# Optimization experiments

Measured on AMD Instinct MI355X. Metric: run time of the kernel, lower is better.

## Reference

```python
import jax, jax.numpy as jnp
import numpy as np

N = 8192
IN_C = 512
OUT_C = 512


def setup_inputs() -> dict:
    key = jax.random.key(0)
    k1, k2, k3 = jax.random.split(key, 3)
    x = jax.random.normal(k1, (N, IN_C), dtype=jnp.float32)
    adj = jax.random.uniform(k2, (N, N), dtype=jnp.float32)
    # torch.rand initializer for the weight (uniform [0,1))
    w = jax.random.uniform(k3, (IN_C, OUT_C), dtype=jnp.float32)
    return {"x": x, "adj": adj, "w": w}


def reference(x, adj, w):
    # A = adj + I
    A = adj + jnp.eye(adj.shape[0], dtype=adj.dtype)
    # D_hat = diag(deg)^{-1/2}; diagonal inverse + sqrt == elementwise rsqrt of degrees
    deg = jnp.sum(A, axis=1)                      # [N]
    d_inv_sqrt = jax.lax.rsqrt(deg)               # [N]
    # A_hat = D_hat @ A @ D_hat == row/col scaling (same math, no dense inverse)
    A_hat = A * d_inv_sqrt[:, None] * d_inv_sqrt[None, :]
    mm_1 = A_hat @ x                              # [N, in_c]
    return jax.nn.elu(mm_1 @ w)                   # [N, out_c]
```

## Files before the change

### kernel.cpp

```cpp
#include <hip/hip_runtime.h>

#define NN 8192
#define CC 512

typedef __attribute__((ext_vector_type(8))) short short8;
typedef __attribute__((ext_vector_type(4))) float f32x4;
typedef unsigned short ushort_t;

__device__ __forceinline__ unsigned short f2bf(float f) {
    unsigned int u = __float_as_uint(f);
    u += 0x7FFF + ((u >> 16) & 1);
    return (unsigned short)(u >> 16);
}

__device__ __forceinline__ void gload_lds16(const void* g, void* l) {
    __builtin_amdgcn_global_load_lds((const __attribute__((address_space(1))) unsigned int*)g,
                                     (__attribute__((address_space(3))) unsigned int*)l,
                                     16, 0, 0);
}

__global__ __launch_bounds__(256) void k_rowsum(const float* __restrict__ adj,
                                                float* __restrict__ ds) {
    int row = blockIdx.x;
    const float4* p = (const float4*)(adj + (size_t)row * NN);
    float s = 0.f;
#pragma unroll
    for (int i = 0; i < 8; ++i) {
        float4 v = p[threadIdx.x + i * 256];
        s += (v.x + v.y) + (v.z + v.w);
    }
#pragma unroll
    for (int off = 32; off > 0; off >>= 1) s += __shfl_down(s, off, 64);
    __shared__ float partial[4];
    int wid = threadIdx.x >> 6;
    int lane = threadIdx.x & 63;
    if (lane == 0) partial[wid] = s;
    __syncthreads();
    if (threadIdx.x == 0) {
        float deg = ((partial[0] + partial[1]) + (partial[2] + partial[3])) + 1.0f;
        ds[row] = rsqrtf(deg);
    }
}

__global__ __launch_bounds__(256) void k_transpose(const float* __restrict__ in,
                                                   ushort_t* __restrict__ out,
                                                   const float* __restrict__ scale,
                                                   int R, int C) {
    __shared__ float tile[64][65];
    int r0 = blockIdx.x * 64, c0 = blockIdx.y * 64;
    int t = threadIdx.x;
    int cl = t & 63;
    int rl0 = t >> 6;
#pragma unroll
    for (int i = 0; i < 16; ++i) {
        int r = rl0 + i * 4;
        float v = in[(size_t)(r0 + r) * C + c0 + cl];
        float sc = scale ? scale[r0 + r] : 1.0f;
        tile[r][cl] = v * sc;
    }
    __syncthreads();
#pragma unroll
    for (int i = 0; i < 16; ++i) {
        int c = rl0 + i * 4;
        int r = cl;
        out[(size_t)(c0 + c) * R + r0 + r] = f2bf(tile[r][c]);
    }
}

template <int MODE>
__global__ __launch_bounds__(256, 4) void k_gemm1(const float* __restrict__ adj,
                                                  const ushort_t* __restrict__ yt,
                                                  const float* __restrict__ ds,
                                                  const float* __restrict__ x,
                                                  ushort_t* __restrict__ mm1,
                                                  float* __restrict__ part) {
    __shared__ __align__(16) ushort_t As[128 * 64];
    __shared__ __align__(16) ushort_t Bs[128 * 64];

    int t = threadIdx.x;
    int wid = t >> 6, lane = t & 63;

    int rowBase, colBase, kt0, ktN, ks;
    if (MODE == 0) {
        int bid = blockIdx.x;
        bid = (bid & 7) * 32 + (bid >> 3);
        colBase = (bid & 3) * 128;
        rowBase = (bid >> 2) * 128;
        kt0 = 0; ktN = NN / 64; ks = 0;
    } else {
        int gid = blockIdx.x;
        int xcd = gid & 7, slot = gid >> 3;
        int cb = slot & 3;
        int g = (slot >> 2) * 8 + xcd;
        int rb = g & 63; ks = g >> 6;
        rowBase = rb * 128; colBase = cb * 128;
        kt0 = ks * (NN / 64 / 4); ktN = kt0 + NN / 64 / 4;
    }

    int ar = t >> 4;
    int ac4 = t & 15;
    const float* aptr = adj + (size_t)(rowBase + ar) * NN + ac4 * 4;

    int brow0 = t >> 3;
    int bs = t & 7;

    float4 areg[8];

    auto loadA = [&](int kt) {
        const float* p = aptr + kt * 64;
#pragma unroll
        for (int i = 0; i < 8; ++i)
            areg[i] = *(const float4*)(p + (size_t)i * 16 * NN);
    };
    auto writeA = [&]() {
#pragma unroll
        for (int i = 0; i < 8; ++i) {
            int row = i * 16 + ar;
            ushort4 u;
            u.x = f2bf(areg[i].x); u.y = f2bf(areg[i].y);
            u.z = f2bf(areg[i].z); u.w = f2bf(areg[i].w);
            *(ushort4*)((char*)As + row * 128 + ((ac4 * 8) ^ ((row & 7) << 4))) = u;
        }
    };
    auto stageB = [&](int kt) {
#pragma unroll
        for (int j = 0; j < 4; ++j) {
            int row = j * 32 + brow0;
            const char* g = (const char*)(yt + (size_t)(colBase + row) * NN + kt * 64 +
                                          ((bs ^ (row & 7)) << 3));
            char* l = (char*)Bs + j * 4096 + wid * 1024;
            gload_lds16(g, l);
        }
    };

    f32x4 acc[4][4] = {};
    int wr = wid >> 1, wc = wid & 1;
    int fr = lane & 15, fq = lane >> 4;

    loadA(kt0);
    for (int kt = kt0; kt < ktN; ++kt) {
        writeA();
        stageB(kt);
        __syncthreads();
        if (kt + 1 < ktN) loadA(kt + 1);
#pragma unroll
        for (int ks2 = 0; ks2 < 2; ++ks2) {
            short8 af[4], bf[4];
#pragma unroll
            for (int m = 0; m < 4; ++m) {
                int row = wr * 64 + m * 16 + fr;
                af[m] = *(const short8*)((const char*)As + row * 128 +
                                         ((ks2 * 64 + fq * 16) ^ ((row & 7) << 4)));
            }
#pragma unroll
            for (int n = 0; n < 4; ++n) {
                int col = wc * 64 + n * 16 + fr;
                bf[n] = *(const short8*)((const char*)Bs + col * 128 +
                                         ((ks2 * 64 + fq * 16) ^ ((col & 7) << 4)));
            }
#pragma unroll
            for (int m = 0; m < 4; ++m)
#pragma unroll
                for (int n = 0; n < 4; ++n)
                    acc[m][n] = __builtin_amdgcn_mfma_f32_16x16x32_bf16(af[m], bf[n], acc[m][n], 0, 0, 0);
        }
        __syncthreads();
    }

#pragma unroll
    for (int m = 0; m < 4; ++m) {
#pragma unroll
        for (int j = 0; j < 4; ++j) {
            int gr = rowBase + wr * 64 + m * 16 + fq * 4 + j;
            float dsr = (MODE == 0) ? ds[gr] : 0.f;
#pragma unroll
            for (int n = 0; n < 4; ++n) {
                int gc = colBase + wc * 64 + n * 16 + fr;
                float p = acc[m][n][j];
                if (MODE == 0) {
                    float v = dsr * (p + dsr * x[(size_t)gr * CC + gc]);
                    mm1[(size_t)gr * CC + gc] = f2bf(v);
                } else if (MODE == 1) {
                    part[((size_t)ks * NN + gr) * CC + gc] = p;
                } else {
                    atomicAdd(&part[(size_t)gr * CC + gc], p);
                }
            }
        }
    }
}

__global__ __launch_bounds__(256) void k_finish(const float* __restrict__ part,
                                                const float* __restrict__ ds,
                                                const float* __restrict__ x,
                                                ushort_t* __restrict__ mm1,
                                                int nsplit) {
    size_t i = (size_t)blockIdx.x * 256 + threadIdx.x;
    const f32x4* p = (const f32x4*)part;
    const size_t stride = (size_t)NN * CC / 4;
    f32x4 s = p[i];
    for (int k = 1; k < nsplit; ++k) s += p[i + (size_t)k * stride];
    int row = (int)(i >> 7);
    float d = ds[row];
    f32x4 xv = ((const f32x4*)x)[i];
    ushort4 u;
    u.x = f2bf(d * (s[0] + d * xv[0]));
    u.y = f2bf(d * (s[1] + d * xv[1]));
    u.z = f2bf(d * (s[2] + d * xv[2]));
    u.w = f2bf(d * (s[3] + d * xv[3]));
    ((ushort4*)mm1)[i] = u;
}

__global__ __launch_bounds__(256, 2) void k_gemm2(const ushort_t* __restrict__ mm1,
                                                  const ushort_t* __restrict__ wt,
                                                  float* __restrict__ out) {
    __shared__ __align__(16) ushort_t As[128 * 64];
    __shared__ __align__(16) ushort_t Bs[128 * 64];

    int t = threadIdx.x;
    int wid = t >> 6, lane = t & 63;
    int bid = blockIdx.x;
    bid = (bid & 7) * 32 + (bid >> 3);
    int cb = bid & 3, rb = bid >> 2;
    int rowBase = rb * 128, colBase = cb * 128;

    int srow0 = t >> 3, ss = t & 7;

    f32x4 acc[4][4] = {};
    int wr = wid >> 1, wc = wid & 1;
    int fr = lane & 15, fq = lane >> 4;

    for (int kt = 0; kt < CC / 64; ++kt) {
#pragma unroll
        for (int j = 0; j < 4; ++j) {
            int row = j * 32 + srow0;
            gload_lds16((const char*)(mm1 + (size_t)(rowBase + row) * CC + kt * 64 +
                                      ((ss ^ (row & 7)) << 3)),
                        (char*)As + j * 4096 + wid * 1024);
            gload_lds16((const char*)(wt + (size_t)(colBase + row) * CC + kt * 64 +
                                      ((ss ^ (row & 7)) << 3)),
                        (char*)Bs + j * 4096 + wid * 1024);
        }
        __syncthreads();
#pragma unroll
        for (int ks = 0; ks < 2; ++ks) {
            short8 af[4], bf[4];
#pragma unroll
            for (int m = 0; m < 4; ++m) {
                int row = wr * 64 + m * 16 + fr;
                af[m] = *(const short8*)((const char*)As + row * 128 +
                                         ((ks * 64 + fq * 16) ^ ((row & 7) << 4)));
            }
#pragma unroll
            for (int n = 0; n < 4; ++n) {
                int col = wc * 64 + n * 16 + fr;
                bf[n] = *(const short8*)((const char*)Bs + col * 128 +
                                         ((ks * 64 + fq * 16) ^ ((col & 7) << 4)));
            }
#pragma unroll
            for (int m = 0; m < 4; ++m)
#pragma unroll
                for (int n = 0; n < 4; ++n)
                    acc[m][n] = __builtin_amdgcn_mfma_f32_16x16x32_bf16(af[m], bf[n], acc[m][n], 0, 0, 0);
        }
        __syncthreads();
    }

#pragma unroll
    for (int m = 0; m < 4; ++m) {
#pragma unroll
        for (int j = 0; j < 4; ++j) {
            int gr = rowBase + wr * 64 + m * 16 + fq * 4 + j;
#pragma unroll
            for (int n = 0; n < 4; ++n) {
                int gc = colBase + wc * 64 + n * 16 + fr;
                float v = acc[m][n][j];
                out[(size_t)gr * CC + gc] = v > 0.f ? v : expm1f(v);
            }
        }
    }
}

extern "C" void kernel_launch(void* const* d_in, const int* in_sizes, int n_in,
                              void* d_out, int out_size, void* d_ws, size_t ws_size,
                              hipStream_t stream) {
    const float* x   = (const float*)d_in[0];
    const float* adj = (const float*)d_in[1];
    const float* w   = (const float*)d_in[2];
    float* out = (float*)d_out;

    char* ws = (char*)d_ws;
    size_t off = 0;
    float*    ds  = (float*)(ws + off);  off += 32u << 10;
    ushort_t* yt  = (ushort_t*)(ws + off);  off += 8u << 20;
    ushort_t* wt  = (ushort_t*)(ws + off);  off += 512u << 10;
    ushort_t* mm1 = (ushort_t*)(ws + off);  off += 8u << 20;
    float*    part = (float*)(ws + off);
    const size_t oneBuf = (size_t)NN * CC * 4;

    k_rowsum<<<NN, 256, 0, stream>>>(adj, ds);
    k_transpose<<<dim3(NN / 64, CC / 64), 256, 0, stream>>>(x, yt, ds, NN, CC);
    k_transpose<<<dim3(CC / 64, CC / 64), 256, 0, stream>>>(w, wt, nullptr, CC, CC);

    if (ws_size >= off + 4 * oneBuf) {
        k_gemm1<1><<<1024, 256, 0, stream>>>(adj, yt, ds, x, mm1, part);
        k_finish<<<NN * CC / 4 / 256, 256, 0, stream>>>(part, ds, x, mm1, 4);
    } else if (ws_size >= off + oneBuf) {
        hipMemsetAsync(part, 0, oneBuf, stream);
        k_gemm1<2><<<1024, 256, 0, stream>>>(adj, yt, ds, x, mm1, part);
        k_finish<<<NN * CC / 4 / 256, 256, 0, stream>>>(part, ds, x, mm1, 1);
    } else {
        k_gemm1<0><<<256, 256, 0, stream>>>(adj, yt, ds, x, mm1, part);
    }

    k_gemm2<<<256, 256, 0, stream>>>(mm1, wt, out);
}
```

Before: 220.5 us.

## Convert adjacency to bf16 during row-sum and stream it via direct LDS loads

The row-sum pass now also writes a bf16 copy of the adjacency matrix. A new split-K GEMM kernel then loads both operands with global_load_lds DMA instead of a register-staged fp32 load, convert and LDS write. This removes the in-loop conversion and register pressure from the main GEMM, but adds an extra 128MB write and a 128MB bf16 re-read on top of the 256MB fp32 read. The atomic fallback path is dropped, and the new path only runs when the workspace can hold the bf16 adjacency.

```diff
diff --git a/kernel.cpp b/kernel.cpp
--- a/kernel.cpp
+++ b/kernel.cpp
@@ -17,6 +17,32 @@
     __builtin_amdgcn_global_load_lds((const __attribute__((address_space(1))) unsigned int*)g,
                                      (__attribute__((address_space(3))) unsigned int*)l,
                                      16, 0, 0);
+}
+
+__global__ __launch_bounds__(256) void k_rowsum_cvt(const float* __restrict__ adj,
+                                                    float* __restrict__ ds,
+                                                    ushort_t* __restrict__ adj16) {
+    int row = blockIdx.x;
+    const float4* p = (const float4*)(adj + (size_t)row * NN);
+    ushort4* q = (ushort4*)(adj16 + (size_t)row * NN);
+    float s = 0.f;
+#pragma unroll
+    for (int i = 0; i < 8; ++i) {
+        float4 v = p[threadIdx.x + i * 256];
+        s += (v.x + v.y) + (v.z + v.w);
+        ushort4 u;
+        u.x = f2bf(v.x); u.y = f2bf(v.y); u.z = f2bf(v.z); u.w = f2bf(v.w);
+        q[threadIdx.x + i * 256] = u;
+    }
+#pragma unroll
+    for (int off = 32; off > 0; off >>= 1) s += __shfl_down(s, off, 64);
+    __shared__ float partial[4];
+    if ((threadIdx.x & 63) == 0) partial[threadIdx.x >> 6] = s;
+    __syncthreads();
+    if (threadIdx.x == 0) {
+        float deg = ((partial[0] + partial[1]) + (partial[2] + partial[3])) + 1.0f;
+        ds[row] = rsqrtf(deg);
+    }
 }
 
 __global__ __launch_bounds__(256) void k_rowsum(const float* __restrict__ adj,
@@ -32,9 +58,7 @@
 #pragma unroll
     for (int off = 32; off > 0; off >>= 1) s += __shfl_down(s, off, 64);
     __shared__ float partial[4];
-    int wid = threadIdx.x >> 6;
-    int lane = threadIdx.x & 63;
-    if (lane == 0) partial[wid] = s;
+    if ((threadIdx.x & 63) == 0) partial[threadIdx.x >> 6] = s;
     __syncthreads();
     if (threadIdx.x == 0) {
         float deg = ((partial[0] + partial[1]) + (partial[2] + partial[3])) + 1.0f;
@@ -64,6 +88,79 @@
         int c = rl0 + i * 4;
         int r = cl;
         out[(size_t)(c0 + c) * R + r0 + r] = f2bf(tile[r][c]);
+    }
+}
+
+__global__ __launch_bounds__(256, 4) void k_gemm1b(const ushort_t* __restrict__ adj16,
+                                                   const ushort_t* __restrict__ yt,
+                                                   float* __restrict__ part) {
+    __shared__ __align__(16) ushort_t As[128 * 64];
+    __shared__ __align__(16) ushort_t Bs[128 * 64];
+
+    int t = threadIdx.x;
+    int wid = t >> 6, lane = t & 63;
+
+    int gid = blockIdx.x;
+    int xcd = gid & 7, slot = gid >> 3;
+    int cb = slot & 3;
+    int g = (slot >> 2) * 8 + xcd;
+    int rb = g & 63, ks = g >> 6;
+    int rowBase = rb * 128, colBase = cb * 128;
+    int kt0 = ks * (NN / 64 / 4), ktN = kt0 + NN / 64 / 4;
+
+    int srow0 = t >> 3, ss = t & 7;
+
+    f32x4 acc[4][4] = {};
+    int wr = wid >> 1, wc = wid & 1;
+    int fr = lane & 15, fq = lane >> 4;
+
+    for (int kt = kt0; kt < ktN; ++kt) {
+#pragma unroll
+        for (int j = 0; j < 4; ++j) {
+            int row = j * 32 + srow0;
+            gload_lds16((const char*)(adj16 + (size_t)(rowBase + row) * NN + kt * 64 +
+                                      ((ss ^ (row & 7)) << 3)),
+                        (char*)As + j * 4096 + wid * 1024);
+            gload_lds16((const char*)(yt + (size_t)(colBase + row) * NN + kt * 64 +
+                                      ((ss ^ (row & 7)) << 3)),
+                        (char*)Bs + j * 4096 + wid * 1024);
+        }
+        __syncthreads();
+#pragma unroll
+        for (int ks2 = 0; ks2 < 2; ++ks2) {
+            short8 af[4], bf[4];
+#pragma unroll
+            for (int m = 0; m < 4; ++m) {
+                int row = wr * 64 + m * 16 + fr;
+                af[m] = *(const short8*)((const char*)As + row * 128 +
+                                         ((ks2 * 64 + fq * 16) ^ ((row & 7) << 4)));
+            }
+#pragma unroll
+            for (int n = 0; n < 4; ++n) {
+                int col = wc * 64 + n * 16 + fr;
+                bf[n] = *(const short8*)((const char*)Bs + col * 128 +
+                                         ((ks2 * 64 + fq * 16) ^ ((col & 7) << 4)));
+            }
+#pragma unroll
+            for (int m = 0; m < 4; ++m)
+#pragma unroll
+                for (int n = 0; n < 4; ++n)
+                    acc[m][n] = __builtin_amdgcn_mfma_f32_16x16x32_bf16(af[m], bf[n], acc[m][n], 0, 0, 0);
+        }
+        __syncthreads();
+    }
+
+#pragma unroll
+    for (int m = 0; m < 4; ++m) {
+#pragma unroll
+        for (int j = 0; j < 4; ++j) {
+            int gr = rowBase + wr * 64 + m * 16 + fq * 4 + j;
+#pragma unroll
+            for (int n = 0; n < 4; ++n) {
+                int gc = colBase + wc * 64 + n * 16 + fr;
+                part[((size_t)ks * NN + gr) * CC + gc] = acc[m][n][j];
+            }
+        }
     }
 }
 
@@ -100,7 +197,6 @@
     int ar = t >> 4;
     int ac4 = t & 15;
     const float* aptr = adj + (size_t)(rowBase + ar) * NN + ac4 * 4;
-
     int brow0 = t >> 3;
     int bs = t & 7;
 
@@ -126,10 +222,9 @@
 #pragma unroll
         for (int j = 0; j < 4; ++j) {
             int row = j * 32 + brow0;
-            const char* g = (const char*)(yt + (size_t)(colBase + row) * NN + kt * 64 +
-                                          ((bs ^ (row & 7)) << 3));
-            char* l = (char*)Bs + j * 4096 + wid * 1024;
-            gload_lds16(g, l);
+            gload_lds16((const char*)(yt + (size_t)(colBase + row) * NN + kt * 64 +
+                                      ((bs ^ (row & 7)) << 3)),
+                        (char*)Bs + j * 4096 + wid * 1024);
         }
     };
 
@@ -180,10 +275,8 @@
                 if (MODE == 0) {
                     float v = dsr * (p + dsr * x[(size_t)gr * CC + gc]);
                     mm1[(size_t)gr * CC + gc] = f2bf(v);
-                } else if (MODE == 1) {
+                } else {
                     part[((size_t)ks * NN + gr) * CC + gc] = p;
-                } else {
-                    atomicAdd(&part[(size_t)gr * CC + gc], p);
                 }
             }
         }
@@ -296,20 +389,26 @@
     ushort_t* wt  = (ushort_t*)(ws + off);  off += 512u << 10;
     ushort_t* mm1 = (ushort_t*)(ws + off);  off += 8u << 20;
     float*    part = (float*)(ws + off);
-    const size_t oneBuf = (size_t)NN * CC * 4;
-
-    k_rowsum<<<NN, 256, 0, stream>>>(adj, ds);
-    k_transpose<<<dim3(NN / 64, CC / 64), 256, 0, stream>>>(x, yt, ds, NN, CC);
-    k_transpose<<<dim3(CC / 64, CC / 64), 256, 0, stream>>>(w, wt, nullptr, CC, CC);
-
-    if (ws_size >= off + 4 * oneBuf) {
+    const size_t partBytes = 4 * (size_t)NN * CC * 4;
+    ushort_t* adj16 = (ushort_t*)(ws + off + partBytes);
+    const size_t adjBytes = (size_t)NN * NN * 2;
+
+    if (ws_size >= off + partBytes + adjBytes) {
+        k_rowsum_cvt<<<NN, 256, 0, stream>>>(adj, ds, adj16);
+        k_transpose<<<dim3(NN / 64, CC / 64), 256, 0, stream>>>(x, yt, ds, NN, CC);
+        k_transpose<<<dim3(CC / 64, CC / 64), 256, 0, stream>>>(w, wt, nullptr, CC, CC);
+        k_gemm1b<<<1024, 256, 0, stream>>>(adj16, yt, part);
+        k_finish<<<NN * CC / 4 / 256, 256, 0, stream>>>(part, ds, x, mm1, 4);
+    } else if (ws_size >= off + partBytes) {
+        k_rowsum<<<NN, 256, 0, stream>>>(adj, ds);
+        k_transpose<<<dim3(NN / 64, CC / 64), 256, 0, stream>>>(x, yt, ds, NN, CC);
+        k_transpose<<<dim3(CC / 64, CC / 64), 256, 0, stream>>>(w, wt, nullptr, CC, CC);
         k_gemm1<1><<<1024, 256, 0, stream>>>(adj, yt, ds, x, mm1, part);
         k_finish<<<NN * CC / 4 / 256, 256, 0, stream>>>(part, ds, x, mm1, 4);
-    } else if (ws_size >= off + oneBuf) {
-        hipMemsetAsync(part, 0, oneBuf, stream);
-        k_gemm1<2><<<1024, 256, 0, stream>>>(adj, yt, ds, x, mm1, part);
-        k_finish<<<NN * CC / 4 / 256, 256, 0, stream>>>(part, ds, x, mm1, 1);
     } else {
+        k_rowsum<<<NN, 256, 0, stream>>>(adj, ds);
+        k_transpose<<<dim3(NN / 64, CC / 64), 256, 0, stream>>>(x, yt, ds, NN, CC);
+        k_transpose<<<dim3(CC / 64, CC / 64), 256, 0, stream>>>(w, wt, nullptr, CC, CC);
         k_gemm1<0><<<256, 256, 0, stream>>>(adj, yt, ds, x, mm1, part);
     }
 
```

Result: slower. 228.8 us (+3.8%).
